# Kernel optimization log

Hardware: AMD Instinct MI355X
Metric: run time of the kernel (lower is better)

The kernel has to match this reference:

```python
import jax, jax.numpy as jnp
import numpy as np

TAU_MEM = 10.0
TAU_SYN = 5.0
REFRACTORY = 2.0
THRESHOLD = 1.0
TRACE_DECAY = 0.95


def setup_inputs() -> dict:
    key = jax.random.key(0)
    k1, k2, k3 = jax.random.split(key, 3)
    T, D, N = 1000, 64, 128
    return {
        "input_signal": jax.random.normal(k1, (T, D), dtype=jnp.float32),
        "input_weights": jax.random.normal(k2, (D, N), dtype=jnp.float32) * 0.1,
        "recurrent_weights": jax.random.normal(k3, (N, N), dtype=jnp.float32) * 0.05,
        "n_timesteps": 1000,
    }


def reference(input_signal, input_weights, recurrent_weights, n_timesteps):
    # Faithful to the torch code: batch_size = input_signal.shape[0] (= T here),
    # and each timestep's input current (1, N) broadcasts across all B rows.
    B = input_signal.shape[0]
    N = input_weights.shape[1]
    dtype = input_signal.dtype
    # Precompute per-step input currents (T, N); valid since n_timesteps == T.
    inp_cur = input_signal[:n_timesteps] @ input_weights

    def step(state, x_t):
        mem, syn, trace, refr = state
        rec = trace @ recurrent_weights                      # (B, N)
        syn = syn * (1.0 - 1.0 / TAU_SYN) + x_t[None, :] + rec
        mem = mem * (1.0 - 1.0 / TAU_MEM) + syn / TAU_MEM
        mem = jnp.where(refr > 0, jnp.zeros_like(mem), mem)  # refractory masking
        refr = jnp.maximum(refr - 1.0, 0.0)
        spikes = (mem > THRESHOLD).astype(dtype)
        mem = mem * (1.0 - spikes)                           # reset on spike
        refr = refr + spikes * REFRACTORY
        trace = trace * TRACE_DECAY + spikes
        return (mem, syn, trace, refr), (spikes, mem)

    z = jnp.zeros((B, N), dtype)
    (_, _, trace, _), (spk, memh) = jax.lax.scan(step, (z, z, z, z), inp_cur)
    spike_trains = jnp.transpose(spk, (1, 0, 2))       # (B, T, N)
    membrane_history = jnp.transpose(memh, (1, 0, 2))  # (B, T, N)
    return spike_trains, membrane_history, trace
```

## Files before the change

### kernel.cpp

```cpp
#include <hip/hip_runtime.h>
#include <math.h>


#define XCHUNK 8
#define NBLK   250

typedef float vf4 __attribute__((ext_vector_type(4)));

__global__ void inpcur_kernel(const float* __restrict__ sig,
                              const float* __restrict__ win,
                              double* __restrict__ inp_cur,
                              int D, int N) {
    const int t = blockIdx.x;
    const int n = threadIdx.x;
    const float* srow = sig + (size_t)t * D;
    double acc = 0.0;
    for (int d = 0; d < D; ++d)
        acc += (double)srow[d] * (double)win[(size_t)d * N + n];
    inp_cur[(size_t)t * N + n] = acc;
}

__global__ __launch_bounds__(64, 1) void simrep_kernel(
    const double* __restrict__ inp_cur,
    const float* __restrict__ wrec,
    float* __restrict__ out,
    long long TN, long long B_TN, int B, int nt) {
    __shared__ float lds_w[128 * 128];

    const int l = threadIdx.x;
    const int j = blockIdx.x;

    __builtin_amdgcn_s_setprio(3);

    float* spk[4];
    float* mem[4];
    bool   wmem[4];
    int    rows[4];
    #pragma unroll
    for (int k = 0; k < 4; ++k) {
        rows[k] = j + k * NBLK;
        spk[k]  = out + (long long)rows[k] * TN;
        mem[k]  = out + B_TN + (long long)rows[k] * TN;
        wmem[k] = (rows[k] != B - 3) && (rows[k] != B - 2);
    }
    float* trace = out + 2 * B_TN;

    {
        const vf4* src = (const vf4*)wrec;
        vf4* dst = (vf4*)lds_w;
        for (int i = 0; i < 64; ++i)
            dst[i * 64 + l] = src[i * 64 + l];
    }

    double mem_lo = 0.0, syn_lo = 0.0, trc_lo = 0.0, refr_lo = 0.0, rec_lo = 0.0;
    double mem_hi = 0.0, syn_hi = 0.0, trc_hi = 0.0, refr_hi = 0.0, rec_hi = 0.0;

    double x_lo[XCHUNK], x_hi[XCHUNK];

    for (int t0 = 0; t0 < nt; t0 += XCHUNK) {
        const int cs = (nt - t0 < XCHUNK) ? (nt - t0) : XCHUNK;
        #pragma unroll
        for (int s = 0; s < XCHUNK; ++s) {
            if (s < cs) {
                x_lo[s] = inp_cur[(size_t)(t0 + s) * 128 + l];
                x_hi[s] = inp_cur[(size_t)(t0 + s) * 128 + l + 64];
            }
        }

        #pragma unroll
        for (int s = 0; s < XCHUNK; ++s) {
            if (s >= cs) break;
            const int t = t0 + s;

            syn_lo = syn_lo * (1.0 - 1.0 / 5.0) + x_lo[s] + rec_lo;
            mem_lo = mem_lo * (1.0 - 1.0 / 10.0) + syn_lo / 10.0;
            if (refr_lo > 0.0) mem_lo = 0.0;
            refr_lo = refr_lo - 1.0;
            if (refr_lo < 0.0) refr_lo = 0.0;
            const bool sp_lo = mem_lo > 1.0;

            syn_hi = syn_hi * (1.0 - 1.0 / 5.0) + x_hi[s] + rec_hi;
            mem_hi = mem_hi * (1.0 - 1.0 / 10.0) + syn_hi / 10.0;
            if (refr_hi > 0.0) mem_hi = 0.0;
            refr_hi = refr_hi - 1.0;
            if (refr_hi < 0.0) refr_hi = 0.0;
            const bool sp_hi = mem_hi > 1.0;

            const unsigned long long m0 = __ballot(sp_lo);
            const unsigned long long m1 = __ballot(sp_hi);

            if (sp_lo) { mem_lo = 0.0; refr_lo += 2.0; }
            trc_lo = trc_lo * 0.95 + (sp_lo ? 1.0 : 0.0);
            if (sp_hi) { mem_hi = 0.0; refr_hi += 2.0; }
            trc_hi = trc_hi * 0.95 + (sp_hi ? 1.0 : 0.0);

            {
                const float s0f = sp_lo ? 1.0f : 0.0f;
                const float s1f = sp_hi ? 1.0f : 0.0f;
                const float m0f = (float)mem_lo;
                const float m1f = (float)mem_hi;
                #pragma unroll
                for (int k = 0; k < 4; ++k) {
                    __builtin_nontemporal_store(s0f, &spk[k][(size_t)t * 128 + l]);
                    __builtin_nontemporal_store(s1f, &spk[k][(size_t)t * 128 + l + 64]);
                    if (wmem[k]) {
                        __builtin_nontemporal_store(m0f, &mem[k][(size_t)t * 128 + l]);
                        __builtin_nontemporal_store(m1f, &mem[k][(size_t)t * 128 + l + 64]);
                    }
                }
            }

            double add_lo = 0.0, add_hi = 0.0;
            #pragma unroll 1
            for (int half = 0; half < 2; ++half) {
                unsigned long long m = half ? m1 : m0;
                const float* wb = lds_w + (half ? (64 * 128) : 0);
                while (m) {
                    int kk[8];
                    bool vv[8];
                    #pragma unroll
                    for (int jj = 0; jj < 8; ++jj) {
                        vv[jj] = (m != 0ull);
                        kk[jj] = m ? (int)__builtin_ctzll(m) : 0;
                        m &= (m - 1ull);
                    }
                    float wl[8], wh[8];
                    #pragma unroll
                    for (int jj = 0; jj < 8; ++jj) {
                        wl[jj] = wb[kk[jj] * 128 + l];
                        wh[jj] = wb[kk[jj] * 128 + l + 64];
                    }
                    #pragma unroll
                    for (int jj = 0; jj < 8; ++jj) {
                        add_lo += vv[jj] ? (double)wl[jj] : 0.0;
                        add_hi += vv[jj] ? (double)wh[jj] : 0.0;
                    }
                }
            }
            rec_lo = rec_lo * 0.95 + add_lo;
            rec_hi = rec_hi * 0.95 + add_hi;
        }
    }

    #pragma unroll
    for (int k = 0; k < 4; ++k) {
        trace[(size_t)rows[k] * 128 + l]      = (float)trc_lo;
        trace[(size_t)rows[k] * 128 + l + 64] = (float)trc_hi;
    }
}

__global__ void fixup_kernel(float* __restrict__ mem_base, long long TN,
                             int rowA, int rowB) {
    const long long tn4 = TN / 4;
    const long long idx = (long long)blockIdx.x * blockDim.x + threadIdx.x;
    if (idx >= 2 * tn4) return;
    const int r = (idx < tn4) ? rowA : rowB;
    const long long i = (idx < tn4) ? idx : idx - tn4;
    const vf4 v = ((const vf4*)mem_base)[i];
    __builtin_nontemporal_store(v, (vf4*)mem_base + (long long)r * tn4 + i);
}

extern "C" void kernel_launch(void* const* d_in, const int* in_sizes, int n_in,
                              void* d_out, int out_size, void* d_ws, size_t ws_size,
                              hipStream_t stream) {
    const float* sig  = (const float*)d_in[0];
    const float* win  = (const float*)d_in[1];
    const float* wrec = (const float*)d_in[2];

    int N = 1;
    while ((long long)N * N < (long long)in_sizes[2]) ++N;
    const int D = in_sizes[1] / N;
    const int B = in_sizes[0] / D;
    const int nt = (int)((((long long)out_size / B) - N) / (2 * N));

    const long long TN   = (long long)nt * N;
    const long long B_TN = (long long)B * TN;

    float* out = (float*)d_out;
    double* inp_cur = (double*)(out + B_TN + (long long)(B - 3) * TN);

    inpcur_kernel<<<nt, N, 0, stream>>>(sig, win, inp_cur, D, N);

    simrep_kernel<<<NBLK, 64, 0, stream>>>(inp_cur, wrec, out,
                                           TN, B_TN, B, nt);

    const long long tn4 = TN / 4;
    fixup_kernel<<<(unsigned)((2 * tn4 + 255) / 256), 256, 0, stream>>>(
        out + B_TN, TN, B - 3, B - 2);
}
```

Measured before the change: 1.951 ms.

## Interleave neuron pairs, store weights as doubles in LDS, pipeline gathers

Each lane now owns the adjacent neurons 2l and 2l+1 instead of l and l+64. This allows 8-byte vector loads of the input current and vector stores of spikes, membrane and trace values. The recurrent weights are converted once to double in LDS, with a zero pad row so that empty slots index harmless zeros. This removes the per-gather float-to-double conversion and the select. The two spike masks are merged into one index stream that is consumed in double-buffered batches of eight, so LDS gathers for the next batch are issued before the current one is summed. The cost is doubled LDS footprint (about 132KB) and more register pressure from the two in-flight weight buffers.

```diff
diff --git a/kernel.cpp b/kernel.cpp
--- a/kernel.cpp
+++ b/kernel.cpp
@@ -5,7 +5,9 @@
 #define XCHUNK 8
 #define NBLK   250
 
-typedef float vf4 __attribute__((ext_vector_type(4)));
+typedef float  vf4 __attribute__((ext_vector_type(4)));
+typedef float  vf2 __attribute__((ext_vector_type(2)));
+typedef double vd2 __attribute__((ext_vector_type(2)));
 
 __global__ void inpcur_kernel(const float* __restrict__ sig,
                               const float* __restrict__ win,
@@ -25,7 +27,7 @@
     const float* __restrict__ wrec,
     float* __restrict__ out,
     long long TN, long long B_TN, int B, int nt) {
-    __shared__ float lds_w[128 * 128];
+    __shared__ double lds_w64[129 * 128];
 
     const int l = threadIdx.x;
     const int j = blockIdx.x;
@@ -47,106 +49,133 @@
 
     {
         const vf4* src = (const vf4*)wrec;
-        vf4* dst = (vf4*)lds_w;
-        for (int i = 0; i < 64; ++i)
-            dst[i * 64 + l] = src[i * 64 + l];
-    }
-
-    double mem_lo = 0.0, syn_lo = 0.0, trc_lo = 0.0, refr_lo = 0.0, rec_lo = 0.0;
-    double mem_hi = 0.0, syn_hi = 0.0, trc_hi = 0.0, refr_hi = 0.0, rec_hi = 0.0;
-
-    double x_lo[XCHUNK], x_hi[XCHUNK];
+        vd2* dst = (vd2*)lds_w64;
+        for (int i = 0; i < 64; ++i) {
+            const vf4 v = src[i * 64 + l];
+            const int e = (i * 64 + l) * 2;
+            vd2 a; a.x = (double)v.x; a.y = (double)v.y;
+            vd2 b; b.x = (double)v.z; b.y = (double)v.w;
+            dst[e]     = a;
+            dst[e + 1] = b;
+        }
+        vd2 z; z.x = 0.0; z.y = 0.0;
+        dst[128 * 64 + l] = z;
+    }
+    const vd2* w64v = (const vd2*)lds_w64;
+
+    double mem0 = 0.0, syn0 = 0.0, trc0 = 0.0, refr0 = 0.0, rec0 = 0.0;
+    double mem1 = 0.0, syn1 = 0.0, trc1 = 0.0, refr1 = 0.0, rec1 = 0.0;
+
+    vd2 xa[XCHUNK];
+
+#define EXTRACT8(kk)                                                     \
+    do {                                                                 \
+        _Pragma("unroll") for (int jj = 0; jj < 8; ++jj) {               \
+            const bool useA = (mA != 0ull);                              \
+            const bool any  = ((mA | mB) != 0ull);                       \
+            const unsigned long long msel = useA ? mA : mB;              \
+            const int tz = (int)__builtin_ctzll(msel ? msel : 1ull);     \
+            kk[jj] = any ? (useA ? 2 * tz : 2 * tz + 1) : 128;           \
+            mA = useA ? (mA & (mA - 1ull)) : mA;                         \
+            mB = (useA || !any) ? mB : (mB & (mB - 1ull));               \
+        }                                                                \
+    } while (0)
+
+#define ISSUE8(kk, W)                                                    \
+    do {                                                                 \
+        _Pragma("unroll") for (int jj = 0; jj < 8; ++jj)                 \
+            W[jj] = w64v[kk[jj] * 64 + l];                               \
+    } while (0)
+
+#define CONSUME8(W)                                                      \
+    do {                                                                 \
+        _Pragma("unroll") for (int jj = 0; jj < 8; ++jj) {               \
+            add0 += W[jj].x;                                             \
+            add1 += W[jj].y;                                             \
+        }                                                                \
+    } while (0)
 
     for (int t0 = 0; t0 < nt; t0 += XCHUNK) {
         const int cs = (nt - t0 < XCHUNK) ? (nt - t0) : XCHUNK;
         #pragma unroll
-        for (int s = 0; s < XCHUNK; ++s) {
-            if (s < cs) {
-                x_lo[s] = inp_cur[(size_t)(t0 + s) * 128 + l];
-                x_hi[s] = inp_cur[(size_t)(t0 + s) * 128 + l + 64];
-            }
-        }
+        for (int s = 0; s < XCHUNK; ++s)
+            if (s < cs)
+                xa[s] = ((const vd2*)(inp_cur + (size_t)(t0 + s) * 128))[l];
 
         #pragma unroll
         for (int s = 0; s < XCHUNK; ++s) {
             if (s >= cs) break;
             const int t = t0 + s;
 
-            syn_lo = syn_lo * (1.0 - 1.0 / 5.0) + x_lo[s] + rec_lo;
-            mem_lo = mem_lo * (1.0 - 1.0 / 10.0) + syn_lo / 10.0;
-            if (refr_lo > 0.0) mem_lo = 0.0;
-            refr_lo = refr_lo - 1.0;
-            if (refr_lo < 0.0) refr_lo = 0.0;
-            const bool sp_lo = mem_lo > 1.0;
-
-            syn_hi = syn_hi * (1.0 - 1.0 / 5.0) + x_hi[s] + rec_hi;
-            mem_hi = mem_hi * (1.0 - 1.0 / 10.0) + syn_hi / 10.0;
-            if (refr_hi > 0.0) mem_hi = 0.0;
-            refr_hi = refr_hi - 1.0;
-            if (refr_hi < 0.0) refr_hi = 0.0;
-            const bool sp_hi = mem_hi > 1.0;
-
-            const unsigned long long m0 = __ballot(sp_lo);
-            const unsigned long long m1 = __ballot(sp_hi);
-
-            if (sp_lo) { mem_lo = 0.0; refr_lo += 2.0; }
-            trc_lo = trc_lo * 0.95 + (sp_lo ? 1.0 : 0.0);
-            if (sp_hi) { mem_hi = 0.0; refr_hi += 2.0; }
-            trc_hi = trc_hi * 0.95 + (sp_hi ? 1.0 : 0.0);
+            syn0 = syn0 * (1.0 - 1.0 / 5.0) + xa[s].x + rec0;
+            mem0 = mem0 * (1.0 - 1.0 / 10.0) + syn0 * 0.1;
+            if (refr0 > 0.0) mem0 = 0.0;
+            refr0 = refr0 - 1.0;
+            if (refr0 < 0.0) refr0 = 0.0;
+            const bool sp0 = mem0 > 1.0;
+
+            syn1 = syn1 * (1.0 - 1.0 / 5.0) + xa[s].y + rec1;
+            mem1 = mem1 * (1.0 - 1.0 / 10.0) + syn1 * 0.1;
+            if (refr1 > 0.0) mem1 = 0.0;
+            refr1 = refr1 - 1.0;
+            if (refr1 < 0.0) refr1 = 0.0;
+            const bool sp1 = mem1 > 1.0;
+
+            unsigned long long mA = __ballot(sp0);
+            unsigned long long mB = __ballot(sp1);
+            const int nb =
+                (int)((__popcll(mA) + __popcll(mB) + 7) >> 3);
+
+            if (sp0) { mem0 = 0.0; refr0 += 2.0; }
+            trc0 = trc0 * 0.95 + (sp0 ? 1.0 : 0.0);
+            if (sp1) { mem1 = 0.0; refr1 += 2.0; }
+            trc1 = trc1 * 0.95 + (sp1 ? 1.0 : 0.0);
+
+            double add0 = 0.0, add1 = 0.0;
+            int kA[8], kB[8];
+            vd2 WA[8], WB[8];
+
+            if (nb) { EXTRACT8(kA); ISSUE8(kA, WA); }
 
             {
-                const float s0f = sp_lo ? 1.0f : 0.0f;
-                const float s1f = sp_hi ? 1.0f : 0.0f;
-                const float m0f = (float)mem_lo;
-                const float m1f = (float)mem_hi;
+                vf2 sv; sv.x = sp0 ? 1.0f : 0.0f; sv.y = sp1 ? 1.0f : 0.0f;
+                vf2 mv; mv.x = (float)mem0; mv.y = (float)mem1;
                 #pragma unroll
                 for (int k = 0; k < 4; ++k) {
-                    __builtin_nontemporal_store(s0f, &spk[k][(size_t)t * 128 + l]);
-                    __builtin_nontemporal_store(s1f, &spk[k][(size_t)t * 128 + l + 64]);
-                    if (wmem[k]) {
-                        __builtin_nontemporal_store(m0f, &mem[k][(size_t)t * 128 + l]);
-                        __builtin_nontemporal_store(m1f, &mem[k][(size_t)t * 128 + l + 64]);
-                    }
+                    __builtin_nontemporal_store(
+                        sv, (vf2*)(spk[k] + (size_t)t * 128) + l);
+                    if (wmem[k])
+                        __builtin_nontemporal_store(
+                            mv, (vf2*)(mem[k] + (size_t)t * 128) + l);
                 }
             }
 
-            double add_lo = 0.0, add_hi = 0.0;
-            #pragma unroll 1
-            for (int half = 0; half < 2; ++half) {
-                unsigned long long m = half ? m1 : m0;
-                const float* wb = lds_w + (half ? (64 * 128) : 0);
-                while (m) {
-                    int kk[8];
-                    bool vv[8];
-                    #pragma unroll
-                    for (int jj = 0; jj < 8; ++jj) {
-                        vv[jj] = (m != 0ull);
-                        kk[jj] = m ? (int)__builtin_ctzll(m) : 0;
-                        m &= (m - 1ull);
-                    }
-                    float wl[8], wh[8];
-                    #pragma unroll
-                    for (int jj = 0; jj < 8; ++jj) {
-                        wl[jj] = wb[kk[jj] * 128 + l];
-                        wh[jj] = wb[kk[jj] * 128 + l + 64];
-                    }
-                    #pragma unroll
-                    for (int jj = 0; jj < 8; ++jj) {
-                        add_lo += vv[jj] ? (double)wl[jj] : 0.0;
-                        add_hi += vv[jj] ? (double)wh[jj] : 0.0;
-                    }
+            if (nb) {
+                const int npair = nb >> 1;
+                #pragma unroll 1
+                for (int p = 0; p < npair; ++p) {
+                    EXTRACT8(kB); ISSUE8(kB, WB);
+                    CONSUME8(WA);
+                    EXTRACT8(kA); ISSUE8(kA, WA);
+                    CONSUME8(WB);
                 }
+                CONSUME8(WA);
             }
-            rec_lo = rec_lo * 0.95 + add_lo;
-            rec_hi = rec_hi * 0.95 + add_hi;
+            rec0 = rec0 * 0.95 + add0;
+            rec1 = rec1 * 0.95 + add1;
         }
     }
 
-    #pragma unroll
-    for (int k = 0; k < 4; ++k) {
-        trace[(size_t)rows[k] * 128 + l]      = (float)trc_lo;
-        trace[(size_t)rows[k] * 128 + l + 64] = (float)trc_hi;
-    }
+    {
+        vf2 tv; tv.x = (float)trc0; tv.y = (float)trc1;
+        #pragma unroll
+        for (int k = 0; k < 4; ++k)
+            ((vf2*)(trace + (size_t)rows[k] * 128))[l] = tv;
+    }
+
+#undef EXTRACT8
+#undef ISSUE8
+#undef CONSUME8
 }
 
 __global__ void fixup_kernel(float* __restrict__ mem_base, long long TN,
```

Result: slower. 2.618 ms (+34.2%).
